# Kernel optimization log

Hardware: AMD Instinct MI355X
Metric: run time of the kernel (lower is better)

## Reference

```python
import jax, jax.numpy as jnp
import numpy as np

N, B, FIN, FOUT = 4096, 16, 128, 128
DENSITY = 0.01


def setup_inputs() -> dict:
    key = jax.random.key(0)
    k1, k2, k3, k4 = jax.random.split(key, 4)
    # sparse binary adjacency (static pattern), stored dense for the reference
    adj = (jax.random.uniform(k1, (N, N)) < DENSITY).astype(jnp.float32)
    x = jax.random.normal(k2, (B, N, FIN), dtype=jnp.float32)
    W = jax.random.normal(k3, (FOUT, FIN), dtype=jnp.float32) * (1.0 / np.sqrt(FIN))
    b = jax.random.normal(k4, (FOUT,), dtype=jnp.float32) * 0.01
    return {"adj": adj, "x": x, "W": W, "b": b}


def _normalized_adj(adj):
    # A_hat = D^{-1/2} (A + I) D^{-1/2}, degrees from column sums (dim=0 in torch)
    a_self = adj + jnp.eye(adj.shape[0], dtype=adj.dtype)
    dinv = jax.lax.rsqrt(jnp.sum(a_self, axis=0))
    return dinv[:, None] * a_self * dinv[None, :]


def reference(adj, x, W, b):
    a_norm = _normalized_adj(adj)
    # SpMM aggregation over nodes: (N,N) x (B,N,F) -> (B,N,F)
    agg = jnp.einsum('nm,bmf->bnf', a_norm, x)
    # dense linear transform: fc(agg)
    return jnp.einsum('bnf,of->bno', agg, W) + b
```

## Files before the change

### kernel.cpp

```cpp
#include <hip/hip_runtime.h>


#define NN 4096
#define FD 128
#define NB 16
#define CAP 96
#define CPAD 104
#define XB 512

typedef float     f32x4 __attribute__((ext_vector_type(4)));
typedef _Float16  f16x8 __attribute__((ext_vector_type(8)));
typedef int       i32x2 __attribute__((ext_vector_type(2)));

#define XR 128
#define XP 136

__global__ __launch_bounds__(256) void k_bx(const float* __restrict__ A,
                                            float* __restrict__ deg,
                                            int* __restrict__ cnt,
                                            unsigned short* __restrict__ csr,
                                            const float* __restrict__ x,
                                            const float* __restrict__ W,
                                            _Float16* __restrict__ y) {
    __shared__ __align__(16) char smem[2 * XR * XP * 2];
    const int t = threadIdx.x;

    if (blockIdx.x < XB) {
        _Float16 (*sX)[XP] = (_Float16(*)[XP])smem;
        _Float16 (*sW)[XP] = (_Float16(*)[XP])(smem + XR * XP * 2);
        const size_t rbase = (size_t)blockIdx.x * XR;

        #pragma unroll
        for (int i = 0; i < 8; ++i) {
            const int id = t + i * 256;
            const int o = id >> 4, f8 = (id & 15) * 8;
            const f32x4 a = *(const f32x4*)&W[(size_t)o * FD + f8];
            const f32x4 b = *(const f32x4*)&W[(size_t)o * FD + f8 + 4];
            f16x8 h;
            h[0]=(_Float16)a.x; h[1]=(_Float16)a.y; h[2]=(_Float16)a.z; h[3]=(_Float16)a.w;
            h[4]=(_Float16)b.x; h[5]=(_Float16)b.y; h[6]=(_Float16)b.z; h[7]=(_Float16)b.w;
            *(f16x8*)&sW[o][f8] = h;
        }
        #pragma unroll
        for (int i = 0; i < 8; ++i) {
            const int id = t + i * 256;
            const int r = id >> 4, f8 = (id & 15) * 8;
            const f32x4 a = *(const f32x4*)&x[(rbase + r) * FD + f8];
            const f32x4 b = *(const f32x4*)&x[(rbase + r) * FD + f8 + 4];
            f16x8 h;
            h[0]=(_Float16)a.x; h[1]=(_Float16)a.y; h[2]=(_Float16)a.z; h[3]=(_Float16)a.w;
            h[4]=(_Float16)b.x; h[5]=(_Float16)b.y; h[6]=(_Float16)b.z; h[7]=(_Float16)b.w;
            *(f16x8*)&sX[r][f8] = h;
        }
        __syncthreads();

        const int w = t >> 6, lane = t & 63;
        const int lrow = lane & 15, koct = (lane >> 4) * 8;
        f32x4 acc[2][8] = {};
        #pragma unroll
        for (int kc = 0; kc < 4; ++kc) {
            const int ko = kc * 32 + koct;
            f16x8 aa0 = *(const f16x8*)&sX[w * 32 + lrow][ko];
            f16x8 aa1 = *(const f16x8*)&sX[w * 32 + 16 + lrow][ko];
            #pragma unroll
            for (int nt = 0; nt < 8; ++nt) {
                const f16x8 bb = *(const f16x8*)&sW[nt * 16 + lrow][ko];
                acc[0][nt] = __builtin_amdgcn_mfma_f32_16x16x32_f16(aa0, bb, acc[0][nt], 0, 0, 0);
                acc[1][nt] = __builtin_amdgcn_mfma_f32_16x16x32_f16(aa1, bb, acc[1][nt], 0, 0, 0);
            }
        }
        #pragma unroll
        for (int mt = 0; mt < 2; ++mt) {
            const size_t row0 = rbase + w * 32 + mt * 16 + (lane >> 4) * 4;
            #pragma unroll
            for (int nt = 0; nt < 8; ++nt) {
                const int col = nt * 16 + (lane & 15);
                #pragma unroll
                for (int r = 0; r < 4; ++r)
                    y[(row0 + r) * FD + col] = (_Float16)acc[mt][nt][r];
            }
        }
        return;
    }

    int* sCnt = (int*)smem;
    const int n = blockIdx.x - XB;
    const float* row = A + (size_t)n * NN + t * 16;
    float r[16];
    *(f32x4*)&r[0]  = ((const f32x4*)row)[0];
    *(f32x4*)&r[4]  = ((const f32x4*)row)[1];
    *(f32x4*)&r[8]  = ((const f32x4*)row)[2];
    *(f32x4*)&r[12] = ((const f32x4*)row)[3];

    int c = 0;
    #pragma unroll
    for (int j = 0; j < 16; ++j) c += (r[j] != 0.0f) ? 1 : 0;
    sCnt[t] = c;
    __syncthreads();
    for (int off = 1; off < 256; off <<= 1) {
        const int v = sCnt[t];
        const int u = (t >= off) ? sCnt[t - off] : 0;
        __syncthreads();
        sCnt[t] = v + u;
        __syncthreads();
    }
    int pos = sCnt[t] - c;
    #pragma unroll
    for (int j = 0; j < 16; ++j) {
        if (r[j] != 0.0f) {
            const int m = t * 16 + j;
            if (pos < CAP) csr[(size_t)n * CAP + pos] = (unsigned short)m;
            ++pos;
            atomicAdd(&deg[m], 1.0f);
        }
    }
    if (t == 255) {
        int tot = sCnt[255];
        cnt[n] = tot < CAP ? tot : CAP;
    }
}

__global__ __launch_bounds__(256) void k_dinv(const float* __restrict__ deg,
                                              float* __restrict__ dinv) {
    const int i = blockIdx.x * 256 + threadIdx.x;
    dinv[i] = rsqrtf(1.0f + deg[i]);
}

__global__ __launch_bounds__(256) void k_agg2(const _Float16* __restrict__ y,
                                              const int* __restrict__ cnt,
                                              const unsigned short* __restrict__ csr,
                                              const float* __restrict__ dinv,
                                              const float* __restrict__ bias,
                                              float* __restrict__ out) {
    __shared__ int sL[4][CPAD * 2];
    const int t = threadIdx.x, w = t >> 6, lane = t & 63;
    const int bid = blockIdx.x;
    const int xcd = bid & 7;
    const int b0  = 2 * xcd;
    const int n   = (bid >> 3) * 4 + w;
    const int c = cnt[n];
    const int totPad = (c + 1 + 3) & ~3;

    for (int k = lane; k < CPAD; k += 64) {
        int m; float wv;
        if (k < c)       { m = csr[(size_t)n * CAP + k]; wv = dinv[m]; }
        else if (k == c) { m = n; wv = dinv[n]; }
        else             { m = n; wv = 0.0f; }
        sL[w][2 * k]     = m << 8;
        sL[w][2 * k + 1] = __float_as_int(wv);
    }
    __syncthreads();

    const int rq = lane >> 4;
    const int fo = (lane & 15) * 16;
    const char* yb0 = (const char*)y + (size_t)b0 * (NN * FD * 2);
    const char* yb1 = yb0 + (size_t)(NN * FD * 2);

    float acc0[8] = {}, acc1[8] = {};
    i32x2 e = *(const i32x2*)&sL[w][2 * rq];
    int voff = e.x + fo;
    f16x8 pA = *(const f16x8*)(yb0 + (size_t)(unsigned)voff);
    f16x8 pB = *(const f16x8*)(yb1 + (size_t)(unsigned)voff);
    float wt = __int_as_float(e.y);
    for (int k = rq + 4; k < totPad; k += 4) {
        const i32x2 e2 = *(const i32x2*)&sL[w][2 * k];
        const int v2 = e2.x + fo;
        const f16x8 nA = *(const f16x8*)(yb0 + (size_t)(unsigned)v2);
        const f16x8 nB = *(const f16x8*)(yb1 + (size_t)(unsigned)v2);
        const float wt2 = __int_as_float(e2.y);
        #pragma unroll
        for (int j = 0; j < 8; ++j) {
            acc0[j] = fmaf(wt, (float)pA[j], acc0[j]);
            acc1[j] = fmaf(wt, (float)pB[j], acc1[j]);
        }
        pA = nA; pB = nB; wt = wt2;
    }
    #pragma unroll
    for (int j = 0; j < 8; ++j) {
        acc0[j] = fmaf(wt, (float)pA[j], acc0[j]);
        acc1[j] = fmaf(wt, (float)pB[j], acc1[j]);
    }

    #pragma unroll
    for (int j = 0; j < 8; ++j) {
        acc0[j] += __shfl_xor(acc0[j], 16);
        acc0[j] += __shfl_xor(acc0[j], 32);
        acc1[j] += __shfl_xor(acc1[j], 16);
        acc1[j] += __shfl_xor(acc1[j], 32);
    }

    if (lane < 32) {
        const float dn = dinv[n];
        const int h = lane >> 4;
        const int f0 = (lane & 15) * 8 + h * 4;
        const f32x4 bb = *(const f32x4*)(bias + f0);
        f32x4 o0, o1;
        o0.x = acc0[h * 4 + 0] * dn + bb.x;
        o0.y = acc0[h * 4 + 1] * dn + bb.y;
        o0.z = acc0[h * 4 + 2] * dn + bb.z;
        o0.w = acc0[h * 4 + 3] * dn + bb.w;
        o1.x = acc1[h * 4 + 0] * dn + bb.x;
        o1.y = acc1[h * 4 + 1] * dn + bb.y;
        o1.z = acc1[h * 4 + 2] * dn + bb.z;
        o1.w = acc1[h * 4 + 3] * dn + bb.w;
        f32x4* d0 = (f32x4*)(out + ((size_t)b0 * NN + n) * FD + f0);
        f32x4* d1 = (f32x4*)(out + ((size_t)(b0 + 1) * NN + n) * FD + f0);
        __builtin_nontemporal_store(o0, d0);
        __builtin_nontemporal_store(o1, d1);
    }
}

extern "C" void kernel_launch(void* const* d_in, const int* in_sizes, int n_in,
                              void* d_out, int out_size, void* d_ws, size_t ws_size,
                              hipStream_t stream) {
    const float* A    = (const float*)d_in[0];
    const float* x    = (const float*)d_in[1];
    const float* W    = (const float*)d_in[2];
    const float* bias = (const float*)d_in[3];
    float* out = (float*)d_out;

    float*          deg  = (float*)d_ws;
    float*          dinv = deg + NN;
    int*            cnt  = (int*)(dinv + NN);
    unsigned short* csr  = (unsigned short*)(cnt + NN);
    _Float16*       y    = (_Float16*)((char*)d_ws + (3 * NN * 4 + (size_t)NN * CAP * 2));

    hipMemsetAsync(deg, 0, NN * sizeof(float), stream);
    k_bx  <<<XB + NN, 256, 0, stream>>>(A, deg, cnt, csr, x, W, y);
    k_dinv<<<NN / 256, 256, 0, stream>>>(deg, dinv);
    k_agg2<<<(NN / 4) * (NB / 2), 256, 0, stream>>>(y, cnt, csr, dinv, bias, out);
}
```

Measured before the change: 77.22 us.

## Fuse dinv into aggregation, load x directly into MFMA regs, vectorize y stores

```diff
diff --git a/kernel.cpp b/kernel.cpp
--- a/kernel.cpp
+++ b/kernel.cpp
@@ -9,10 +9,10 @@
 #define XB 512
 
 typedef float     f32x4 __attribute__((ext_vector_type(4)));
+typedef _Float16  f16x4 __attribute__((ext_vector_type(4)));
 typedef _Float16  f16x8 __attribute__((ext_vector_type(8)));
 typedef int       i32x2 __attribute__((ext_vector_type(2)));
 
-#define XR 128
 #define XP 136
 
 __global__ __launch_bounds__(256) void k_bx(const float* __restrict__ A,
@@ -22,13 +22,12 @@
                                             const float* __restrict__ x,
                                             const float* __restrict__ W,
                                             _Float16* __restrict__ y) {
-    __shared__ __align__(16) char smem[2 * XR * XP * 2];
+    __shared__ __align__(16) char smem[FD * XP * 2];
     const int t = threadIdx.x;
 
     if (blockIdx.x < XB) {
-        _Float16 (*sX)[XP] = (_Float16(*)[XP])smem;
-        _Float16 (*sW)[XP] = (_Float16(*)[XP])(smem + XR * XP * 2);
-        const size_t rbase = (size_t)blockIdx.x * XR;
+        _Float16 (*sW)[XP] = (_Float16(*)[XP])smem;
+        const size_t rbase = (size_t)blockIdx.x * 128;
 
         #pragma unroll
         for (int i = 0; i < 8; ++i) {
@@ -41,43 +40,43 @@
             h[4]=(_Float16)b.x; h[5]=(_Float16)b.y; h[6]=(_Float16)b.z; h[7]=(_Float16)b.w;
             *(f16x8*)&sW[o][f8] = h;
         }
-        #pragma unroll
-        for (int i = 0; i < 8; ++i) {
-            const int id = t + i * 256;
-            const int r = id >> 4, f8 = (id & 15) * 8;
-            const f32x4 a = *(const f32x4*)&x[(rbase + r) * FD + f8];
-            const f32x4 b = *(const f32x4*)&x[(rbase + r) * FD + f8 + 4];
-            f16x8 h;
-            h[0]=(_Float16)a.x; h[1]=(_Float16)a.y; h[2]=(_Float16)a.z; h[3]=(_Float16)a.w;
-            h[4]=(_Float16)b.x; h[5]=(_Float16)b.y; h[6]=(_Float16)b.z; h[7]=(_Float16)b.w;
-            *(f16x8*)&sX[r][f8] = h;
-        }
         __syncthreads();
 
         const int w = t >> 6, lane = t & 63;
         const int lrow = lane & 15, koct = (lane >> 4) * 8;
+        const float* xr0 = x + (rbase + w * 32 + lrow) * FD;
+        const float* xr1 = xr0 + 16 * FD;
         f32x4 acc[2][8] = {};
         #pragma unroll
         for (int kc = 0; kc < 4; ++kc) {
             const int ko = kc * 32 + koct;
-            f16x8 aa0 = *(const f16x8*)&sX[w * 32 + lrow][ko];
-            f16x8 aa1 = *(const f16x8*)&sX[w * 32 + 16 + lrow][ko];
+            const f32x4 a0 = *(const f32x4*)&xr0[ko];
+            const f32x4 a1 = *(const f32x4*)&xr0[ko + 4];
+            const f32x4 b0 = *(const f32x4*)&xr1[ko];
+            const f32x4 b1 = *(const f32x4*)&xr1[ko + 4];
+            f16x8 xx0, xx1;
+            xx0[0]=(_Float16)a0.x; xx0[1]=(_Float16)a0.y; xx0[2]=(_Float16)a0.z; xx0[3]=(_Float16)a0.w;
+            xx0[4]=(_Float16)a1.x; xx0[5]=(_Float16)a1.y; xx0[6]=(_Float16)a1.z; xx0[7]=(_Float16)a1.w;
+            xx1[0]=(_Float16)b0.x; xx1[1]=(_Float16)b0.y; xx1[2]=(_Float16)b0.z; xx1[3]=(_Float16)b0.w;
+            xx1[4]=(_Float16)b1.x; xx1[5]=(_Float16)b1.y; xx1[6]=(_Float16)b1.z; xx1[7]=(_Float16)b1.w;
             #pragma unroll
-            for (int nt = 0; nt < 8; ++nt) {
-                const f16x8 bb = *(const f16x8*)&sW[nt * 16 + lrow][ko];
-                acc[0][nt] = __builtin_amdgcn_mfma_f32_16x16x32_f16(aa0, bb, acc[0][nt], 0, 0, 0);
-                acc[1][nt] = __builtin_amdgcn_mfma_f32_16x16x32_f16(aa1, bb, acc[1][nt], 0, 0, 0);
+            for (int ot = 0; ot < 8; ++ot) {
+                const f16x8 ww = *(const f16x8*)&sW[ot * 16 + lrow][ko];
+                acc[0][ot] = __builtin_amdgcn_mfma_f32_16x16x32_f16(ww, xx0, acc[0][ot], 0, 0, 0);
+                acc[1][ot] = __builtin_amdgcn_mfma_f32_16x16x32_f16(ww, xx1, acc[1][ot], 0, 0, 0);
             }
         }
         #pragma unroll
-        for (int mt = 0; mt < 2; ++mt) {
-            const size_t row0 = rbase + w * 32 + mt * 16 + (lane >> 4) * 4;
+        for (int rt = 0; rt < 2; ++rt) {
+            const size_t row = rbase + w * 32 + rt * 16 + (lane & 15);
             #pragma unroll
-            for (int nt = 0; nt < 8; ++nt) {
-                const int col = nt * 16 + (lane & 15);
-                #pragma unroll
-                for (int r = 0; r < 4; ++r)
-                    y[(row0 + r) * FD + col] = (_Float16)acc[mt][nt][r];
+            for (int ot = 0; ot < 8; ++ot) {
+                f16x4 h;
+                h[0] = (_Float16)acc[rt][ot][0];
+                h[1] = (_Float16)acc[rt][ot][1];
+                h[2] = (_Float16)acc[rt][ot][2];
+                h[3] = (_Float16)acc[rt][ot][3];
+                *(f16x4*)&y[row * FD + ot * 16 + (lane >> 4) * 4] = h;
             }
         }
         return;
@@ -120,16 +119,10 @@
     }
 }
 
-__global__ __launch_bounds__(256) void k_dinv(const float* __restrict__ deg,
-                                              float* __restrict__ dinv) {
-    const int i = blockIdx.x * 256 + threadIdx.x;
-    dinv[i] = rsqrtf(1.0f + deg[i]);
-}
-
 __global__ __launch_bounds__(256) void k_agg2(const _Float16* __restrict__ y,
                                               const int* __restrict__ cnt,
                                               const unsigned short* __restrict__ csr,
-                                              const float* __restrict__ dinv,
+                                              const float* __restrict__ deg,
                                               const float* __restrict__ bias,
                                               float* __restrict__ out) {
     __shared__ int sL[4][CPAD * 2];
@@ -143,8 +136,8 @@
 
     for (int k = lane; k < CPAD; k += 64) {
         int m; float wv;
-        if (k < c)       { m = csr[(size_t)n * CAP + k]; wv = dinv[m]; }
-        else if (k == c) { m = n; wv = dinv[n]; }
+        if (k < c)       { m = csr[(size_t)n * CAP + k]; wv = rsqrtf(1.0f + deg[m]); }
+        else if (k == c) { m = n; wv = rsqrtf(1.0f + deg[n]); }
         else             { m = n; wv = 0.0f; }
         sL[w][2 * k]     = m << 8;
         sL[w][2 * k + 1] = __float_as_int(wv);
@@ -158,15 +151,15 @@
 
     float acc0[8] = {}, acc1[8] = {};
     i32x2 e = *(const i32x2*)&sL[w][2 * rq];
-    int voff = e.x + fo;
-    f16x8 pA = *(const f16x8*)(yb0 + (size_t)(unsigned)voff);
-    f16x8 pB = *(const f16x8*)(yb1 + (size_t)(unsigned)voff);
+    unsigned voff = (unsigned)(e.x + fo);
+    f16x8 pA = *(const f16x8*)(yb0 + voff);
+    f16x8 pB = *(const f16x8*)(yb1 + voff);
     float wt = __int_as_float(e.y);
     for (int k = rq + 4; k < totPad; k += 4) {
         const i32x2 e2 = *(const i32x2*)&sL[w][2 * k];
-        const int v2 = e2.x + fo;
-        const f16x8 nA = *(const f16x8*)(yb0 + (size_t)(unsigned)v2);
-        const f16x8 nB = *(const f16x8*)(yb1 + (size_t)(unsigned)v2);
+        const unsigned v2 = (unsigned)(e2.x + fo);
+        const f16x8 nA = *(const f16x8*)(yb0 + v2);
+        const f16x8 nB = *(const f16x8*)(yb1 + v2);
         const float wt2 = __int_as_float(e2.y);
         #pragma unroll
         for (int j = 0; j < 8; ++j) {
@@ -190,7 +183,7 @@
     }
 
     if (lane < 32) {
-        const float dn = dinv[n];
+        const float dn = rsqrtf(1.0f + deg[n]);
         const int h = lane >> 4;
         const int f0 = (lane & 15) * 8 + h * 4;
         const f32x4 bb = *(const f32x4*)(bias + f0);
@@ -220,13 +213,11 @@
     float* out = (float*)d_out;
 
     float*          deg  = (float*)d_ws;
-    float*          dinv = deg + NN;
-    int*            cnt  = (int*)(dinv + NN);
+    int*            cnt  = (int*)((char*)d_ws + 2 * NN * 4);
     unsigned short* csr  = (unsigned short*)(cnt + NN);
     _Float16*       y    = (_Float16*)((char*)d_ws + (3 * NN * 4 + (size_t)NN * CAP * 2));
 
     hipMemsetAsync(deg, 0, NN * sizeof(float), stream);
     k_bx  <<<XB + NN, 256, 0, stream>>>(A, deg, cnt, csr, x, W, y);
-    k_dinv<<<NN / 256, 256, 0, stream>>>(deg, dinv);
-    k_agg2<<<(NN / 4) * (NB / 2), 256, 0, stream>>>(y, cnt, csr, dinv, bias, out);
+    k_agg2<<<(NN / 4) * (NB / 2), 256, 0, stream>>>(y, cnt, csr, deg, bias, out);
 }
```

Result: no change. 75.92 us (-1.7%).
